# Kernel optimization log

Hardware: AMD Instinct MI355X
Metric: run time of the kernel (lower is better)

Reference implementation:

```python
import jax, jax.numpy as jnp
import numpy as np

B, C, H, W = 8, 256, 64, 64
K = 3                      # kernel size
DG = 4                     # deformable groups
PAD = (K - 1) // 2
K2 = K * K
GN_GROUPS = 32
EPS = 1e-5


def setup_inputs() -> dict:
    key = jax.random.key(0)
    ks = jax.random.split(key, 6)
    x = jax.random.normal(ks[0], (B, C, H, W), dtype=jnp.float32)
    shape = jax.random.normal(ks[1], (B, 4, H, W), dtype=jnp.float32)
    # 1x1 offset conv weight [dg*k*k*2, 4] (bias=False); small std keeps offsets sane
    w_offset = jax.random.normal(ks[2], (DG * K2 * 2, 4), dtype=jnp.float32) * 0.1
    # deformable conv weight [out_c, in_c, K, K]
    w_deform = jax.random.normal(ks[3], (C, C, K, K), dtype=jnp.float32) * 0.01
    gamma = jnp.ones((C,), dtype=jnp.float32)
    beta = jnp.zeros((C,), dtype=jnp.float32)
    return {"x": x, "shape": shape, "w_offset": w_offset,
            "w_deform": w_deform, "gamma": gamma, "beta": beta}


def _bilinear_sample(img, py, px):
    # img: [Cg, H, W]; py, px: [K2, H, W] absolute sampling coords
    h, w = img.shape[1], img.shape[2]
    y0 = jnp.floor(py)
    x0 = jnp.floor(px)
    ly = py - y0
    lx = px - x0

    def gather(yi, xi):
        valid = ((yi >= 0) & (yi <= h - 1) & (xi >= 0) & (xi <= w - 1)).astype(img.dtype)
        yc = jnp.clip(yi, 0, h - 1).astype(jnp.int32)
        xc = jnp.clip(xi, 0, w - 1).astype(jnp.int32)
        return img[:, yc, xc] * valid  # [Cg, K2, H, W]

    v00 = gather(y0, x0)
    v01 = gather(y0, x0 + 1)
    v10 = gather(y0 + 1, x0)
    v11 = gather(y0 + 1, x0 + 1)
    return (v00 * (1 - ly) * (1 - lx) + v01 * (1 - ly) * lx
            + v10 * ly * (1 - lx) + v11 * ly * lx)


def _forward(x, shape, w_offset, w_deform, gamma, beta):
    # offset = 1x1 conv on shape (detached in torch): [B, DG*K2*2, H, W]
    offset = jnp.einsum('oc,bchw->bohw', w_offset, shape)
    # mmcv layout: per group, per kernel position, (dy, dx)
    off = offset.reshape(B, DG, K2, 2, H, W)
    dy, dx = off[:, :, :, 0], off[:, :, :, 1]  # [B, DG, K2, H, W]

    ki = (jnp.arange(K2) // K - PAD).astype(jnp.float32)  # kernel row offsets
    kj = (jnp.arange(K2) % K - PAD).astype(jnp.float32)
    ys = jnp.arange(H, dtype=jnp.float32)
    xs = jnp.arange(W, dtype=jnp.float32)
    # absolute sampling positions [B, DG, K2, H, W]
    py = dy + ki[None, None, :, None, None] + ys[None, None, None, :, None]
    px = dx + kj[None, None, :, None, None] + xs[None, None, None, None, :]

    cg = C // DG
    x_g = x.reshape(B, DG, cg, H, W)
    # sampled: [B, DG, Cg, K2, H, W]
    sampled = jax.vmap(jax.vmap(_bilinear_sample))(x_g, py, px)

    w = w_deform.reshape(C, DG, cg, K2)
    out = jnp.einsum('bgckhw,ogck->bohw', sampled, w)  # [B, C, H, W]

    # GroupNorm(32, C) + ReLU
    og = out.reshape(B, GN_GROUPS, C // GN_GROUPS, H, W)
    mu = og.mean(axis=(2, 3, 4), keepdims=True)
    var = og.var(axis=(2, 3, 4), keepdims=True)
    norm = ((og - mu) * jax.lax.rsqrt(var + EPS)).reshape(B, C, H, W)
    y = norm * gamma[None, :, None, None] + beta[None, :, None, None]
    return jax.nn.relu(y)


def reference(x, shape, w_offset, w_deform, gamma, beta):
    return _forward(x, shape, w_offset, w_deform, gamma, beta)
```

## Files before the change

### kernel.cpp

```cpp
#include <hip/hip_runtime.h>
#include <hip/hip_bf16.h>

#define EPSV 1e-5f

typedef __attribute__((ext_vector_type(8))) short short8;
typedef __attribute__((ext_vector_type(4))) float f32x4;
typedef __attribute__((ext_vector_type(2))) float f32x2;
typedef __attribute__((ext_vector_type(4))) unsigned u32x4;

#define W2_BYTES 1179648ull

__global__ __launch_bounds__(256) void wt2_kernel(const float* __restrict__ wd,
                                                  __hip_bfloat16* __restrict__ w2,
                                                  float* __restrict__ st) {
  int idx = blockIdx.x * 256 + threadIdx.x;
  float v = wd[idx];
  int o   = idx / 2304;
  int rem = idx - o * 2304;
  int cin = rem / 9;
  int k   = rem - cin * 9;
  int p   = cin >> 5;
  int c   = cin & 31;
  w2[o * 2304 + p * 288 + k * 32 + c] = __float2bfloat16(v);
  if (idx < 512) st[idx] = 0.f;
}

static __device__ __forceinline__ f32x2 unpk(unsigned u) {
  union { unsigned i; float f; } lo, hi;
  lo.i = u << 16;
  hi.i = u & 0xffff0000u;
  return (f32x2){lo.f, hi.f};
}

static __device__ __forceinline__ unsigned pkbf(float a, float b) {
  __hip_bfloat162 p = __float22bfloat162_rn(make_float2(a, b));
  return *(unsigned*)&p;
}

__global__ __launch_bounds__(512, 2) void fused_kernel(
    const float* __restrict__ x, const float* __restrict__ shp,
    const float* __restrict__ woff, const __hip_bfloat16* __restrict__ w2,
    float* __restrict__ out, float* __restrict__ st) {
  __shared__ __align__(16) unsigned short sX[2][8 * 64 * 32];
  __shared__ __align__(16) unsigned short sB[2][128 * 64];
  __shared__ float sW[288];

  const int b    = blockIdx.x & 7;
  const int band = blockIdx.x >> 3;
  const int h0   = band << 1;
  const int t    = threadIdx.x;
  const int wv   = t >> 6, lane = t & 63;
  const int quad = lane >> 4, l15 = lane & 15;

  const float* xb = x + ((size_t)b << 20);
  const unsigned short* w2b = (const unsigned short*)w2;

  if (t < 288) sW[t] = woff[t];

  if (wv < 4) {
    const int cw = wv;
    const unsigned short* aro =
        w2b + (size_t)((cw << 6) + l15) * 2304 + (quad << 3);

    f32x4 acc[4][8];
#pragma unroll
    for (int mo = 0; mo < 4; ++mo)
#pragma unroll
      for (int np = 0; np < 8; ++np) acc[mo][np] = (f32x4){0.f, 0.f, 0.f, 0.f};

    short8 afc[2][4];
#pragma unroll
    for (int ks = 0; ks < 2; ++ks)
#pragma unroll
      for (int mo = 0; mo < 4; ++mo)
        afc[ks][mo] = *(const short8*)(aro + (size_t)(mo << 4) * 2304 + (ks << 5));

    asm volatile("s_waitcnt lgkmcnt(0)" ::: "memory");
    asm volatile("s_barrier" ::: "memory");
    asm volatile("s_barrier" ::: "memory");

    for (int it = 0; it < 36; ++it) {
      const unsigned short* Bc = sB[it & 1];
#pragma unroll
      for (int np = 0; np < 8; ++np) {
        const int row = (np << 4) + l15;
#pragma unroll
        for (int ks = 0; ks < 2; ++ks) {
          short8 bf = *(const short8*)&Bc[(row << 6) +
                         ((((ks << 2) + quad) ^ (row & 7)) << 3)];
#pragma unroll
          for (int mo = 0; mo < 4; ++mo)
            acc[mo][np] = __builtin_amdgcn_mfma_f32_16x16x32_bf16(afc[ks][mo], bf, acc[mo][np], 0, 0, 0);
        }
      }
      if (it < 35) {
#pragma unroll
        for (int ks = 0; ks < 2; ++ks)
#pragma unroll
          for (int mo = 0; mo < 4; ++mo)
            afc[ks][mo] = *(const short8*)(aro + (size_t)(mo << 4) * 2304 +
                                           (size_t)((it + 1) << 6) + (ks << 5));
      }
      asm volatile("s_barrier" ::: "memory");
    }

#pragma unroll
    for (int mo = 0; mo < 4; ++mo) {
      float s = 0.f, q = 0.f;
#pragma unroll
      for (int np = 0; np < 8; ++np)
#pragma unroll
        for (int r = 0; r < 4; ++r) { float v = acc[mo][np][r]; s += v; q += v * v; }
#pragma unroll
      for (int m = 1; m < 16; m <<= 1) { s += __shfl_xor(s, m, 64); q += __shfl_xor(q, m, 64); }
      if (l15 == 0) {
        int gid = (b << 5) + (cw << 3) + (mo << 1) + (quad >> 1);
        atomicAdd(&st[gid], s);
        atomicAdd(&st[256 + gid], q);
      }
    }

    float* ob = out + (((size_t)((b << 8) + (cw << 6))) << 12) + (band << 7);
#pragma unroll
    for (int mo = 0; mo < 4; ++mo)
#pragma unroll
      for (int np = 0; np < 8; ++np)
#pragma unroll
        for (int r = 0; r < 4; ++r)
          ob[((size_t)((mo << 4) + (quad << 2) + r) << 12) + (np << 4) + l15] = acc[mo][np][r];
  } else {
    const int pid     = t - 256;
    const int pxn     = pid & 127;
    const int tapslot = pid >> 7;
    const int pxl     = pxn & 63;
    const int h       = h0 + (pxn >> 6);
    const int spx     = pid & 63;
    const int sc8     = (pid >> 6) & 3;
    const int wslot   = (sc8 ^ ((spx >> 1) & 3)) << 3;

    float a0 = shp[((size_t)(b * 4 + 0) << 12) + (h << 6) + pxl];
    float a1 = shp[((size_t)(b * 4 + 1) << 12) + (h << 6) + pxl];
    float a2 = shp[((size_t)(b * 4 + 2) << 12) + (h << 6) + pxl];
    float a3 = shp[((size_t)(b * 4 + 3) << 12) + (h << 6) + pxl];

    {
      const float* xph = xb + ((size_t)(sc8 << 3) << 12) + spx;
#pragma unroll
      for (int j = 0; j < 8; ++j) {
        const int grow = min(max(h0 - 3 + j, 0), 63);
        float v[8];
#pragma unroll
        for (int jj = 0; jj < 8; ++jj) v[jj] = xph[(jj << 12) + (grow << 6)];
        *(u32x4*)&sX[0][((((j << 6) + spx) << 5)) + wslot] =
            (u32x4){pkbf(v[0], v[1]), pkbf(v[2], v[3]), pkbf(v[4], v[5]), pkbf(v[6], v[7])};
      }
    }

    auto produce = [&](int g, int buf) {
      const int ph  = (g * 57) >> 9;
      const int tap = g - ph * 9;
      const int kr  = (tap * 11) >> 5;
      const int kc  = tap - kr * 3;
      const float* wp = &sW[(((ph >> 1) * 9 + tap)) << 3];
      float dy = wp[0]*a0 + wp[1]*a1 + wp[2]*a2 + wp[3]*a3;
      float dx = wp[4]*a0 + wp[5]*a1 + wp[6]*a2 + wp[7]*a3;
      float py  = dy + (float)(h + kr - 1);
      float pxp = dx + (float)(pxl + kc - 1);
      float y0f = floorf(py), x0f = floorf(pxp);
      float ly = py - y0f, lx = pxp - x0f;
      int y0 = (int)y0f, x0 = (int)x0f;
      float m_y0 = (y0 >=  0 && y0 <= 63) ? 1.f : 0.f;
      float m_y1 = (y0 >= -1 && y0 <= 62) ? 1.f : 0.f;
      float m_x0 = (x0 >=  0 && x0 <= 63) ? 1.f : 0.f;
      float m_x1 = (x0 >= -1 && x0 <= 62) ? 1.f : 0.f;
      float w00 = (1.f - ly) * (1.f - lx) * m_y0 * m_x0;
      float w01 = (1.f - ly) * lx         * m_y0 * m_x1;
      float w10 = ly         * (1.f - lx) * m_y1 * m_x0;
      float w11 = ly         * lx         * m_y1 * m_x1;
      int yc0 = min(max(y0, 0), 63),     yc1 = min(max(y0 + 1, 0), 63);
      int xc0 = min(max(x0, 0), 63),     xc1 = min(max(x0 + 1, 0), 63);
      int ry0 = min(max(yc0 - (h0 - 3), 0), 7);
      int ry1 = min(max(yc1 - (h0 - 3), 0), 7);
      const unsigned short* Xc = sX[ph & 1];
      const int z0 = (xc0 >> 1) & 3, z1 = (xc1 >> 1) & 3;
      const int e00 = ((ry0 << 6) + xc0) << 5, e01 = ((ry0 << 6) + xc1) << 5;
      const int e10 = ((ry1 << 6) + xc0) << 5, e11 = ((ry1 << 6) + xc1) << 5;
      uint4 Av[4], Bv[4], Cv[4], Dv[4];
#pragma unroll
      for (int j = 0; j < 4; ++j) {
        Av[j] = *(const uint4*)&Xc[e00 + ((j ^ z0) << 3)];
        Bv[j] = *(const uint4*)&Xc[e01 + ((j ^ z1) << 3)];
        Cv[j] = *(const uint4*)&Xc[e10 + ((j ^ z0) << 3)];
        Dv[j] = *(const uint4*)&Xc[e11 + ((j ^ z1) << 3)];
      }
#pragma unroll
      for (int j = 0; j < 4; ++j) {
        unsigned ua[4] = {Av[j].x, Av[j].y, Av[j].z, Av[j].w};
        unsigned ub[4] = {Bv[j].x, Bv[j].y, Bv[j].z, Bv[j].w};
        unsigned uc[4] = {Cv[j].x, Cv[j].y, Cv[j].z, Cv[j].w};
        unsigned ud[4] = {Dv[j].x, Dv[j].y, Dv[j].z, Dv[j].w};
        unsigned ov[4];
#pragma unroll
        for (int q = 0; q < 4; ++q) {
          f32x2 v = unpk(ua[q]) * w00 + unpk(ub[q]) * w01
                  + unpk(uc[q]) * w10 + unpk(ud[q]) * w11;
          ov[q] = pkbf(v.x, v.y);
        }
        *(u32x4*)&sB[buf][(pxn << 6) + ((((tapslot << 2) + j) ^ (pxn & 7)) << 3)] =
            (u32x4){ov[0], ov[1], ov[2], ov[3]};
      }
    };

    asm volatile("s_waitcnt lgkmcnt(0)" ::: "memory");
    asm volatile("s_barrier" ::: "memory");

    produce(tapslot, 0);
    asm volatile("s_waitcnt lgkmcnt(0)" ::: "memory");
    asm volatile("s_barrier" ::: "memory");

    for (int it = 0; it < 36; ++it) {
      int s = -1, r0 = 0, nr = 0;
      if (it <= 2) { s = 1; r0 = it * 3; nr = (it == 2) ? 2 : 3; }
      else if (it >= 4 && it <= 29) {
        const int u = it - 4;
        const int pair = (u * 57) >> 9;
        const int v = u - pair * 9;
        if (v < 4)      { s = 2 + (pair << 1); r0 = v << 1; nr = 2; }
        else if (v < 8) { s = 3 + (pair << 1); r0 = (v - 4) << 1; nr = 2; }
      }
      float xr[3][8];
      if (s > 0) {
        const float* xph = xb + ((size_t)((s << 5) + (sc8 << 3)) << 12) + spx;
#pragma unroll
        for (int rr = 0; rr < 3; ++rr)
          if (rr < nr) {
            const int grow = min(max(h0 - 3 + r0 + rr, 0), 63);
#pragma unroll
            for (int jj = 0; jj < 8; ++jj) xr[rr][jj] = xph[(jj << 12) + (grow << 6)];
          }
      }
      if (it < 35) produce(((it + 1) << 1) + tapslot, (it + 1) & 1);
      if (s > 0) {
#pragma unroll
        for (int rr = 0; rr < 3; ++rr)
          if (rr < nr) {
            *(u32x4*)&sX[s & 1][((((r0 + rr) << 6) + spx) << 5) + wslot] =
                (u32x4){pkbf(xr[rr][0], xr[rr][1]), pkbf(xr[rr][2], xr[rr][3]),
                        pkbf(xr[rr][4], xr[rr][5]), pkbf(xr[rr][6], xr[rr][7])};
          }
      }
      asm volatile("s_waitcnt lgkmcnt(0)" ::: "memory");
      asm volatile("s_barrier" ::: "memory");
    }
  }
}

__global__ __launch_bounds__(256) void norm_kernel(float* __restrict__ o,
    const float* __restrict__ st, const float* __restrict__ gamma,
    const float* __restrict__ beta) {
  int idx = blockIdx.x * 256 + threadIdx.x;
  f32x4* p = (f32x4*)o;
  int c = (idx >> 10) & 255;
  int b = idx >> 18;
  int g = b * 32 + (c >> 3);
  const float invn = 1.f / 32768.f;
  float mu  = st[g] * invn;
  float var = st[256 + g] * invn - mu * mu;
  float ga = gamma[c] * rsqrtf(var + EPSV);
  float be = beta[c] - mu * ga;
  f32x4 v = p[idx];
  v.x = fmaxf(fmaf(v.x, ga, be), 0.f);
  v.y = fmaxf(fmaf(v.y, ga, be), 0.f);
  v.z = fmaxf(fmaf(v.z, ga, be), 0.f);
  v.w = fmaxf(fmaf(v.w, ga, be), 0.f);
  __builtin_nontemporal_store(v, &p[idx]);
}

extern "C" void kernel_launch(void* const* d_in, const int* in_sizes, int n_in,
                              void* d_out, int out_size, void* d_ws, size_t ws_size,
                              hipStream_t stream) {
  const float* x     = (const float*)d_in[0];
  const float* shp   = (const float*)d_in[1];
  const float* woff  = (const float*)d_in[2];
  const float* wdef  = (const float*)d_in[3];
  const float* gamma = (const float*)d_in[4];
  const float* beta  = (const float*)d_in[5];
  float* out = (float*)d_out;
  __hip_bfloat16* w2 = (__hip_bfloat16*)d_ws;
  float* st          = (float*)((char*)d_ws + W2_BYTES);

  hipLaunchKernelGGL(wt2_kernel,   dim3(2304), dim3(256), 0, stream, wdef, w2, st);
  hipLaunchKernelGGL(fused_kernel, dim3(256),  dim3(512), 0, stream, x, shp, woff, w2, out, st);
  hipLaunchKernelGGL(norm_kernel,  dim3(8192), dim3(256), 0, stream, out, st, gamma, beta);
}
```

Before: 179.7 us.

## Shift global x staging and a quarter of im2col production onto MFMA waves

Work is rebalanced between the warp-specialized wave groups. The MFMA (consumer) waves now do the global-memory loads of x rows into the sX ring buffer and produce one of the four 8-channel chunks of each bilinear-sampled B tile. The producer waves keep only three chunks. The aim is to stop the producer waves from being the critical path while the MFMA waves sit idle at barriers. The cost is more register pressure and extra issue work on the MFMA waves, which may slow their matrix pipeline.

```diff
diff --git a/kernel.cpp b/kernel.cpp
--- a/kernel.cpp
+++ b/kernel.cpp
@@ -59,6 +59,19 @@
 
   if (wv < 4) {
     const int cw = wv;
+    const int pxn     = t & 127;
+    const int tapslot = t >> 7;
+    const int pxl     = pxn & 63;
+    const int h       = h0 + (pxn >> 6);
+    const int spx   = t & 63;
+    const int sc8   = (t >> 6) & 3;
+    const int wslot = (sc8 ^ ((spx >> 1) & 3)) << 3;
+
+    float a0 = shp[((size_t)(b * 4 + 0) << 12) + (h << 6) + pxl];
+    float a1 = shp[((size_t)(b * 4 + 1) << 12) + (h << 6) + pxl];
+    float a2 = shp[((size_t)(b * 4 + 2) << 12) + (h << 6) + pxl];
+    float a3 = shp[((size_t)(b * 4 + 3) << 12) + (h << 6) + pxl];
+
     const unsigned short* aro =
         w2b + (size_t)((cw << 6) + l15) * 2304 + (quad << 3);
 
@@ -75,11 +88,80 @@
       for (int mo = 0; mo < 4; ++mo)
         afc[ks][mo] = *(const short8*)(aro + (size_t)(mo << 4) * 2304 + (ks << 5));
 
+    auto produceC = [&](int g, int buf) {
+      const int ph  = (g * 57) >> 9;
+      const int tap = g - ph * 9;
+      const int kr  = (tap * 11) >> 5;
+      const int kc  = tap - kr * 3;
+      const float* wp = &sW[(((ph >> 1) * 9 + tap)) << 3];
+      float dy = wp[0]*a0 + wp[1]*a1 + wp[2]*a2 + wp[3]*a3;
+      float dx = wp[4]*a0 + wp[5]*a1 + wp[6]*a2 + wp[7]*a3;
+      float py  = dy + (float)(h + kr - 1);
+      float pxp = dx + (float)(pxl + kc - 1);
+      float y0f = floorf(py), x0f = floorf(pxp);
+      float ly = py - y0f, lx = pxp - x0f;
+      int y0 = (int)y0f, x0 = (int)x0f;
+      float m_y0 = (y0 >=  0 && y0 <= 63) ? 1.f : 0.f;
+      float m_y1 = (y0 >= -1 && y0 <= 62) ? 1.f : 0.f;
+      float m_x0 = (x0 >=  0 && x0 <= 63) ? 1.f : 0.f;
+      float m_x1 = (x0 >= -1 && x0 <= 62) ? 1.f : 0.f;
+      float w00 = (1.f - ly) * (1.f - lx) * m_y0 * m_x0;
+      float w01 = (1.f - ly) * lx         * m_y0 * m_x1;
+      float w10 = ly         * (1.f - lx) * m_y1 * m_x0;
+      float w11 = ly         * lx         * m_y1 * m_x1;
+      int yc0 = min(max(y0, 0), 63),     yc1 = min(max(y0 + 1, 0), 63);
+      int xc0 = min(max(x0, 0), 63),     xc1 = min(max(x0 + 1, 0), 63);
+      int ry0 = min(max(yc0 - (h0 - 3), 0), 7);
+      int ry1 = min(max(yc1 - (h0 - 3), 0), 7);
+      const unsigned short* Xc = sX[ph & 1];
+      const int z0 = (xc0 >> 1) & 3, z1 = (xc1 >> 1) & 3;
+      uint4 Au = *(const uint4*)&Xc[(((ry0 << 6) + xc0) << 5) + ((3 ^ z0) << 3)];
+      uint4 Bu = *(const uint4*)&Xc[(((ry0 << 6) + xc1) << 5) + ((3 ^ z1) << 3)];
+      uint4 Cu = *(const uint4*)&Xc[(((ry1 << 6) + xc0) << 5) + ((3 ^ z0) << 3)];
+      uint4 Du = *(const uint4*)&Xc[(((ry1 << 6) + xc1) << 5) + ((3 ^ z1) << 3)];
+      unsigned ua[4] = {Au.x, Au.y, Au.z, Au.w};
+      unsigned ub[4] = {Bu.x, Bu.y, Bu.z, Bu.w};
+      unsigned uc[4] = {Cu.x, Cu.y, Cu.z, Cu.w};
+      unsigned ud[4] = {Du.x, Du.y, Du.z, Du.w};
+      unsigned ov[4];
+#pragma unroll
+      for (int q = 0; q < 4; ++q) {
+        f32x2 v = unpk(ua[q]) * w00 + unpk(ub[q]) * w01
+                + unpk(uc[q]) * w10 + unpk(ud[q]) * w11;
+        ov[q] = pkbf(v.x, v.y);
+      }
+      *(u32x4*)&sB[buf][(pxn << 6) + ((((tapslot << 2) + 3) ^ (pxn & 7)) << 3)] =
+          (u32x4){ov[0], ov[1], ov[2], ov[3]};
+    };
+
     asm volatile("s_waitcnt lgkmcnt(0)" ::: "memory");
     asm volatile("s_barrier" ::: "memory");
+
+    produceC(tapslot, 0);
+    asm volatile("s_waitcnt lgkmcnt(0)" ::: "memory");
     asm volatile("s_barrier" ::: "memory");
 
     for (int it = 0; it < 36; ++it) {
+      int s = -1, r0 = 0, nr = 0;
+      if (it <= 2) { s = 1; r0 = it * 3; nr = (it == 2) ? 2 : 3; }
+      else if (it >= 4 && it <= 29) {
+        const int u = it - 4;
+        const int pair = (u * 57) >> 9;
+        const int v = u - pair * 9;
+        if (v < 4)      { s = 2 + (pair << 1); r0 = v << 1; nr = 2; }
+        else if (v < 8) { s = 3 + (pair << 1); r0 = (v - 4) << 1; nr = 2; }
+      }
+      float xr[3][8];
+      if (s > 0) {
+        const float* xph = xb + ((size_t)((s << 5) + (sc8 << 3)) << 12) + spx;
+#pragma unroll
+        for (int rr = 0; rr < 3; ++rr)
+          if (rr < nr) {
+            const int grow = min(max(h0 - 3 + r0 + rr, 0), 63);
+#pragma unroll
+            for (int jj = 0; jj < 8; ++jj) xr[rr][jj] = xph[(jj << 12) + (grow << 6)];
+          }
+      }
       const unsigned short* Bc = sB[it & 1];
 #pragma unroll
       for (int np = 0; np < 8; ++np) {
@@ -100,7 +182,18 @@
           for (int mo = 0; mo < 4; ++mo)
             afc[ks][mo] = *(const short8*)(aro + (size_t)(mo << 4) * 2304 +
                                            (size_t)((it + 1) << 6) + (ks << 5));
-      }
+        produceC(((it + 1) << 1) + tapslot, (it + 1) & 1);
+      }
+      if (s > 0) {
+#pragma unroll
+        for (int rr = 0; rr < 3; ++rr)
+          if (rr < nr) {
+            *(u32x4*)&sX[s & 1][((((r0 + rr) << 6) + spx) << 5) + wslot] =
+                (u32x4){pkbf(xr[rr][0], xr[rr][1]), pkbf(xr[rr][2], xr[rr][3]),
+                        pkbf(xr[rr][4], xr[rr][5]), pkbf(xr[rr][6], xr[rr][7])};
+          }
+      }
+      asm volatile("s_waitcnt lgkmcnt(0)" ::: "memory");
       asm volatile("s_barrier" ::: "memory");
     }
 
@@ -185,16 +278,16 @@
       const int z0 = (xc0 >> 1) & 3, z1 = (xc1 >> 1) & 3;
       const int e00 = ((ry0 << 6) + xc0) << 5, e01 = ((ry0 << 6) + xc1) << 5;
       const int e10 = ((ry1 << 6) + xc0) << 5, e11 = ((ry1 << 6) + xc1) << 5;
-      uint4 Av[4], Bv[4], Cv[4], Dv[4];
-#pragma unroll
-      for (int j = 0; j < 4; ++j) {
+      uint4 Av[3], Bv[3], Cv[3], Dv[3];
+#pragma unroll
+      for (int j = 0; j < 3; ++j) {
         Av[j] = *(const uint4*)&Xc[e00 + ((j ^ z0) << 3)];
         Bv[j] = *(const uint4*)&Xc[e01 + ((j ^ z1) << 3)];
         Cv[j] = *(const uint4*)&Xc[e10 + ((j ^ z0) << 3)];
         Dv[j] = *(const uint4*)&Xc[e11 + ((j ^ z1) << 3)];
       }
 #pragma unroll
-      for (int j = 0; j < 4; ++j) {
+      for (int j = 0; j < 3; ++j) {
         unsigned ua[4] = {Av[j].x, Av[j].y, Av[j].z, Av[j].w};
         unsigned ub[4] = {Bv[j].x, Bv[j].y, Bv[j].z, Bv[j].w};
         unsigned uc[4] = {Cv[j].x, Cv[j].y, Cv[j].z, Cv[j].w};
@@ -219,36 +312,7 @@
     asm volatile("s_barrier" ::: "memory");
 
     for (int it = 0; it < 36; ++it) {
-      int s = -1, r0 = 0, nr = 0;
-      if (it <= 2) { s = 1; r0 = it * 3; nr = (it == 2) ? 2 : 3; }
-      else if (it >= 4 && it <= 29) {
-        const int u = it - 4;
-        const int pair = (u * 57) >> 9;
-        const int v = u - pair * 9;
-        if (v < 4)      { s = 2 + (pair << 1); r0 = v << 1; nr = 2; }
-        else if (v < 8) { s = 3 + (pair << 1); r0 = (v - 4) << 1; nr = 2; }
-      }
-      float xr[3][8];
-      if (s > 0) {
-        const float* xph = xb + ((size_t)((s << 5) + (sc8 << 3)) << 12) + spx;
-#pragma unroll
-        for (int rr = 0; rr < 3; ++rr)
-          if (rr < nr) {
-            const int grow = min(max(h0 - 3 + r0 + rr, 0), 63);
-#pragma unroll
-            for (int jj = 0; jj < 8; ++jj) xr[rr][jj] = xph[(jj << 12) + (grow << 6)];
-          }
-      }
       if (it < 35) produce(((it + 1) << 1) + tapslot, (it + 1) & 1);
-      if (s > 0) {
-#pragma unroll
-        for (int rr = 0; rr < 3; ++rr)
-          if (rr < nr) {
-            *(u32x4*)&sX[s & 1][((((r0 + rr) << 6) + spx) << 5) + wslot] =
-                (u32x4){pkbf(xr[rr][0], xr[rr][1]), pkbf(xr[rr][2], xr[rr][3]),
-                        pkbf(xr[rr][4], xr[rr][5]), pkbf(xr[rr][6], xr[rr][7])};
-          }
-      }
       asm volatile("s_waitcnt lgkmcnt(0)" ::: "memory");
       asm volatile("s_barrier" ::: "memory");
     }
```

Result: slower. 187.9 us (+4.6%).

## Prefetch producer x-rows one round ahead, raise producer priority, use packed FMA

Applied to the files above, without the earlier changes.

The producer warps now issue global loads for the next round's x rows before the current round's produce step. The loaded values are held in ping-pong register arrays and committed to LDS one round later, so global load latency is hidden across a barrier. Producer waves also get raised scheduling priority via s_setprio, and the bilinear blend is rewritten as chained elementwise FMAs on float2. These changes cost extra registers for the second staging buffer, which may hurt occupancy or cause spills.

```diff
diff --git a/kernel.cpp b/kernel.cpp
--- a/kernel.cpp
+++ b/kernel.cpp
@@ -129,6 +129,7 @@
         for (int r = 0; r < 4; ++r)
           ob[((size_t)((mo << 4) + (quad << 2) + r) << 12) + (np << 4) + l15] = acc[mo][np][r];
   } else {
+    __builtin_amdgcn_s_setprio(1);
     const int pid     = t - 256;
     const int pxn     = pid & 127;
     const int tapslot = pid >> 7;
@@ -155,6 +156,43 @@
             (u32x4){pkbf(v[0], v[1]), pkbf(v[2], v[3]), pkbf(v[4], v[5]), pkbf(v[6], v[7])};
       }
     }
+
+    auto sched = [&](int r, int& s, int& r0, int& nr) {
+      s = -1; r0 = 0; nr = 0;
+      if (r <= 2) { s = 1; r0 = r * 3; nr = (r == 2) ? 2 : 3; }
+      else if (r >= 4 && r <= 29) {
+        const int u = r - 4;
+        const int pair = (u * 57) >> 9;
+        const int v = u - pair * 9;
+        if (v < 4)      { s = 2 + (pair << 1); r0 = v << 1; nr = 2; }
+        else if (v < 8) { s = 3 + (pair << 1); r0 = (v - 4) << 1; nr = 2; }
+      }
+    };
+    auto issueS = [&](int r, float (&xr)[3][8]) {
+      int s, r0, nr; sched(r, s, r0, nr);
+      if (s > 0) {
+        const float* xph = xb + ((size_t)((s << 5) + (sc8 << 3)) << 12) + spx;
+#pragma unroll
+        for (int rr = 0; rr < 3; ++rr)
+          if (rr < nr) {
+            const int grow = min(max(h0 - 3 + r0 + rr, 0), 63);
+#pragma unroll
+            for (int jj = 0; jj < 8; ++jj) xr[rr][jj] = xph[(jj << 12) + (grow << 6)];
+          }
+      }
+    };
+    auto commitS = [&](int r, float (&xr)[3][8]) {
+      int s, r0, nr; sched(r, s, r0, nr);
+      if (s > 0) {
+#pragma unroll
+        for (int rr = 0; rr < 3; ++rr)
+          if (rr < nr) {
+            *(u32x4*)&sX[s & 1][((((r0 + rr) << 6) + spx) << 5) + wslot] =
+                (u32x4){pkbf(xr[rr][0], xr[rr][1]), pkbf(xr[rr][2], xr[rr][3]),
+                        pkbf(xr[rr][4], xr[rr][5]), pkbf(xr[rr][6], xr[rr][7])};
+          }
+      }
+    };
 
     auto produce = [&](int g, int buf) {
       const int ph  = (g * 57) >> 9;
@@ -177,6 +215,8 @@
       float w01 = (1.f - ly) * lx         * m_y0 * m_x1;
       float w10 = ly         * (1.f - lx) * m_y1 * m_x0;
       float w11 = ly         * lx         * m_y1 * m_x1;
+      const f32x2 w00v = {w00, w00}, w01v = {w01, w01};
+      const f32x2 w10v = {w10, w10}, w11v = {w11, w11};
       int yc0 = min(max(y0, 0), 63),     yc1 = min(max(y0 + 1, 0), 63);
       int xc0 = min(max(x0, 0), 63),     xc1 = min(max(x0 + 1, 0), 63);
       int ry0 = min(max(yc0 - (h0 - 3), 0), 7);
@@ -193,64 +233,45 @@
         Cv[j] = *(const uint4*)&Xc[e10 + ((j ^ z0) << 3)];
         Dv[j] = *(const uint4*)&Xc[e11 + ((j ^ z1) << 3)];
       }
+#define BL(UA, UB, UC, UD)                                                    \
+      ({ f32x2 v_ = __builtin_elementwise_fma(unpk(UA), w00v,                 \
+                    __builtin_elementwise_fma(unpk(UB), w01v,                 \
+                    __builtin_elementwise_fma(unpk(UC), w10v,                 \
+                                              unpk(UD) * w11v)));             \
+         pkbf(v_.x, v_.y); })
 #pragma unroll
       for (int j = 0; j < 4; ++j) {
-        unsigned ua[4] = {Av[j].x, Av[j].y, Av[j].z, Av[j].w};
-        unsigned ub[4] = {Bv[j].x, Bv[j].y, Bv[j].z, Bv[j].w};
-        unsigned uc[4] = {Cv[j].x, Cv[j].y, Cv[j].z, Cv[j].w};
-        unsigned ud[4] = {Dv[j].x, Dv[j].y, Dv[j].z, Dv[j].w};
-        unsigned ov[4];
-#pragma unroll
-        for (int q = 0; q < 4; ++q) {
-          f32x2 v = unpk(ua[q]) * w00 + unpk(ub[q]) * w01
-                  + unpk(uc[q]) * w10 + unpk(ud[q]) * w11;
-          ov[q] = pkbf(v.x, v.y);
-        }
+        unsigned o0 = BL(Av[j].x, Bv[j].x, Cv[j].x, Dv[j].x);
+        unsigned o1 = BL(Av[j].y, Bv[j].y, Cv[j].y, Dv[j].y);
+        unsigned o2 = BL(Av[j].z, Bv[j].z, Cv[j].z, Dv[j].z);
+        unsigned o3 = BL(Av[j].w, Bv[j].w, Cv[j].w, Dv[j].w);
         *(u32x4*)&sB[buf][(pxn << 6) + ((((tapslot << 2) + j) ^ (pxn & 7)) << 3)] =
-            (u32x4){ov[0], ov[1], ov[2], ov[3]};
-      }
+            (u32x4){o0, o1, o2, o3};
+      }
+#undef BL
     };
 
     asm volatile("s_waitcnt lgkmcnt(0)" ::: "memory");
     asm volatile("s_barrier" ::: "memory");
 
+    float xrA[3][8], xrB[3][8];
+    issueS(0, xrA);
     produce(tapslot, 0);
     asm volatile("s_waitcnt lgkmcnt(0)" ::: "memory");
     asm volatile("s_barrier" ::: "memory");
 
-    for (int it = 0; it < 36; ++it) {
-      int s = -1, r0 = 0, nr = 0;
-      if (it <= 2) { s = 1; r0 = it * 3; nr = (it == 2) ? 2 : 3; }
-      else if (it >= 4 && it <= 29) {
-        const int u = it - 4;
-        const int pair = (u * 57) >> 9;
-        const int v = u - pair * 9;
-        if (v < 4)      { s = 2 + (pair << 1); r0 = v << 1; nr = 2; }
-        else if (v < 8) { s = 3 + (pair << 1); r0 = (v - 4) << 1; nr = 2; }
-      }
-      float xr[3][8];
-      if (s > 0) {
-        const float* xph = xb + ((size_t)((s << 5) + (sc8 << 3)) << 12) + spx;
-#pragma unroll
-        for (int rr = 0; rr < 3; ++rr)
-          if (rr < nr) {
-            const int grow = min(max(h0 - 3 + r0 + rr, 0), 63);
-#pragma unroll
-            for (int jj = 0; jj < 8; ++jj) xr[rr][jj] = xph[(jj << 12) + (grow << 6)];
-          }
-      }
-      if (it < 35) produce(((it + 1) << 1) + tapslot, (it + 1) & 1);
-      if (s > 0) {
-#pragma unroll
-        for (int rr = 0; rr < 3; ++rr)
-          if (rr < nr) {
-            *(u32x4*)&sX[s & 1][((((r0 + rr) << 6) + spx) << 5) + wslot] =
-                (u32x4){pkbf(xr[rr][0], xr[rr][1]), pkbf(xr[rr][2], xr[rr][3]),
-                        pkbf(xr[rr][4], xr[rr][5]), pkbf(xr[rr][6], xr[rr][7])};
-          }
-      }
+    auto round = [&](int it, float (&xrIss)[3][8], float (&xrCom)[3][8]) {
+      if (it < 35) {
+        issueS(it + 1, xrIss);
+        produce(((it + 1) << 1) + tapslot, (it + 1) & 1);
+      }
+      commitS(it, xrCom);
       asm volatile("s_waitcnt lgkmcnt(0)" ::: "memory");
       asm volatile("s_barrier" ::: "memory");
+    };
+    for (int r2 = 0; r2 < 18; ++r2) {
+      round(r2 * 2,     xrB, xrA);
+      round(r2 * 2 + 1, xrA, xrB);
     }
   }
 }
```

New measurement: 182.3 us. No clear change (+1.5%).
